# Optimization experiments

Measured on AMD Instinct MI355X. Metric: run time of the kernel, lower is better.

Reference implementation:

```python
import jax, jax.numpy as jnp
import numpy as np

B, N, D, H = 2, 2048, 1024, 16
DH = D // H  # 64 per-head dim before LRPE
EPS = 1e-5


def setup_inputs() -> dict:
    key = jax.random.key(0)
    ks = jax.random.split(key, 8)
    x = jax.random.normal(ks[0], (B, N, D), dtype=jnp.float32)
    context = jax.random.normal(ks[1], (B, N, D), dtype=jnp.float32)
    Wqkvu = jax.random.normal(ks[2], (4 * D, D), dtype=jnp.float32) * 0.02
    bqkvu = jax.random.normal(ks[3], (4 * D,), dtype=jnp.float32) * 0.02
    Wout = jax.random.normal(ks[4], (D, D), dtype=jnp.float32) * 0.02
    bout = jax.random.normal(ks[5], (D,), dtype=jnp.float32) * 0.02
    # Lrpe theta: 10000**(-2/d * arange(d)) reshaped to (H, 1, DH)
    theta = (10000.0 ** (-2.0 / D * jnp.arange(D, dtype=jnp.float32))).reshape(H, 1, DH)
    ln_w = jnp.ones((D,), dtype=jnp.float32)
    ln_b = jnp.zeros((D,), dtype=jnp.float32)
    return {"x": x, "context": context, "Wqkvu": Wqkvu, "bqkvu": bqkvu,
            "Wout": Wout, "bout": bout, "theta": theta, "ln_w": ln_w, "ln_b": ln_b}


def _lrpe(t, theta, n):
    # t: [b,h,n,d]; theta: [h,1,d]; index: [1,n,1]
    idx = jnp.arange(n, dtype=t.dtype).reshape(1, n, 1)
    th = theta * idx  # [h,n,d]
    return jnp.concatenate([t * jnp.cos(th), t * jnp.sin(th)], axis=-1)  # [b,h,n,2d]


def reference(x, context, Wqkvu, bqkvu, Wout, bout, theta, ln_w, ln_b):
    b, n, d = x.shape
    qkvu = x @ Wqkvu.T + bqkvu  # [b,n,4d]
    q, k, v, u = jnp.split(qkvu, 4, axis=-1)
    tohead = lambda t: t.reshape(b, n, H, DH).transpose(0, 2, 1, 3)  # b h n d
    q, k, v = tohead(q), tohead(k), tohead(v)
    q = jax.nn.silu(q)
    k = jax.nn.silu(k)
    q = _lrpe(q, theta, n)  # [b,h,n,2*DH]
    k = _lrpe(k, theta, n)
    # left form: materialize qk then contract with v
    qk = jnp.einsum('bhmd,bhnd->bhmn', q, k)
    out = jnp.einsum('bhmn,bhne->bhme', qk, v)  # [b,h,n,DH]
    out = out.transpose(0, 2, 1, 3).reshape(b, n, d)
    # LayerNorm
    mu = jnp.mean(out, axis=-1, keepdims=True)
    var = jnp.var(out, axis=-1, keepdims=True)
    out = (out - mu) * jax.lax.rsqrt(var + EPS) * ln_w + ln_b
    out = u * out
    return out @ Wout.T + bout
```

## Files before the change

kernel.cpp:

```cpp
#include <hip/hip_runtime.h>
#include <math.h>

#define B_ 2
#define N_ 2048
#define D_ 1024
#define H_ 16
#define DH_ 64
#define ROWS (B_*N_)
#define FOURD (4*D_)
#define EPS_ 1e-5f

typedef short bf16x8 __attribute__((ext_vector_type(8)));
typedef float f32x4  __attribute__((ext_vector_type(4)));

__device__ __forceinline__ unsigned short f2bf(float f) {
    unsigned int x = __float_as_uint(f);
    unsigned int r = (x + 0x7fffu + ((x >> 16) & 1u)) >> 16;
    return (unsigned short)r;
}

__global__ __launch_bounds__(256)
void cast_f32_bf16(const float* __restrict__ in, unsigned short* __restrict__ out, int n4)
{
    int i = blockIdx.x * 256 + threadIdx.x;
    if (i >= n4) return;
    float4 v = ((const float4*)in)[i];
    ushort4 o;
    o.x = f2bf(v.x); o.y = f2bf(v.y); o.z = f2bf(v.z); o.w = f2bf(v.w);
    ((ushort4*)out)[i] = o;
}

__global__ __launch_bounds__(256)
void gemm_bt_mfma(const unsigned short* __restrict__ A,
                  const unsigned short* __restrict__ Bw,
                  const float* __restrict__ bias, float* __restrict__ C,
                  int M, int N, int K, int siluLim)
{
    __shared__ unsigned short As[128 * 32];
    __shared__ unsigned short Bs[128 * 32];

    const int tid  = threadIdx.x;
    const int row0 = blockIdx.y * 128;
    const int col0 = blockIdx.x * 128;
    const int wave = tid >> 6;
    const int lane = tid & 63;
    const int wr   = (wave >> 1) * 64;
    const int wc   = (wave & 1) * 64;
    const int l15  = lane & 15;
    const int quad = lane >> 4;

    f32x4 acc[4][4] = {};

    const int srow = tid >> 2;
    const int skk  = (tid & 3) * 8;
    const unsigned short* ag = A  + (size_t)(row0 + srow) * K + skk;
    const unsigned short* bg = Bw + (size_t)(col0 + srow) * K + skk;

    typedef const __attribute__((address_space(1))) unsigned int* gp_t;
    typedef __attribute__((address_space(3))) unsigned int* lp_t;
    lp_t asd = (lp_t)(void*)&As[tid * 8];
    lp_t bsd = (lp_t)(void*)&Bs[tid * 8];

    for (int k0 = 0; k0 < K; k0 += 32) {
        __builtin_amdgcn_global_load_lds((gp_t)(const void*)(ag + k0),                asd,        16, 0, 0);
        __builtin_amdgcn_global_load_lds((gp_t)(const void*)(ag + (size_t)64*K + k0), asd + 1024, 16, 0, 0);
        __builtin_amdgcn_global_load_lds((gp_t)(const void*)(bg + k0),                bsd,        16, 0, 0);
        __builtin_amdgcn_global_load_lds((gp_t)(const void*)(bg + (size_t)64*K + k0), bsd + 1024, 16, 0, 0);
        __syncthreads();

        bf16x8 af[4], bfr[4];
#pragma unroll
        for (int i = 0; i < 4; ++i)
            af[i] = *(const bf16x8*)&As[(wr + i * 16 + l15) * 32 + quad * 8];
#pragma unroll
        for (int j = 0; j < 4; ++j)
            bfr[j] = *(const bf16x8*)&Bs[(wc + j * 16 + l15) * 32 + quad * 8];
#pragma unroll
        for (int i = 0; i < 4; ++i)
#pragma unroll
            for (int j = 0; j < 4; ++j)
                acc[i][j] = __builtin_amdgcn_mfma_f32_16x16x32_bf16(af[i], bfr[j], acc[i][j], 0, 0, 0);
        __syncthreads();
    }

#pragma unroll
    for (int i = 0; i < 4; ++i) {
        const int r0 = row0 + wr + i * 16 + quad * 4;
#pragma unroll
        for (int j = 0; j < 4; ++j) {
            const int c = col0 + wc + j * 16 + l15;
            const float bb = bias[c];
#pragma unroll
            for (int r = 0; r < 4; ++r) {
                float v = acc[i][j][r] + bb;
                if (c < siluLim) v = v / (1.f + expf(-v));
                C[(size_t)(r0 + r) * N + c] = v;
            }
        }
    }
}

__global__ __launch_bounds__(256)
void kv_mfma(const float* __restrict__ qkvu, const float* __restrict__ theta,
             float* __restrict__ part)
{
    __shared__ unsigned short kl_s[128][136];
    __shared__ unsigned short v_s [64][136];

    const int bid   = blockIdx.x;
    const int chunk = bid & 15;
    const int bh    = bid >> 4;
    const int h     = bh & 15;
    const int b     = bh >> 4;
    const int tid   = threadIdx.x;
    const int lane  = tid & 63;
    const int wave  = tid >> 6;
    const int l15   = lane & 15;
    const int quad  = lane >> 4;
    const int n0    = chunk * 128;

    for (int i = tid; i < 2048; i += 256) {
        const int nn  = i >> 4;
        const int dh0 = (i & 15) * 4;
        const int n   = n0 + nn;
        const float* qrow = qkvu + (size_t)(b * N_ + n) * FOURD;
        float4 k4 = *(const float4*)(qrow + D_     + h * DH_ + dh0);
        float4 v4 = *(const float4*)(qrow + 2 * D_ + h * DH_ + dh0);
        float kk[4] = {k4.x, k4.y, k4.z, k4.w};
        float vv[4] = {v4.x, v4.y, v4.z, v4.w};
#pragma unroll
        for (int j = 0; j < 4; ++j) {
            const int dh = dh0 + j;
            float s, c; sincosf(theta[h * DH_ + dh] * (float)n, &s, &c);
            kl_s[dh][nn]      = f2bf(kk[j] * c);
            kl_s[64 + dh][nn] = f2bf(kk[j] * s);
            v_s[dh][nn]       = f2bf(vv[j]);
        }
    }
    __syncthreads();

    f32x4 acc[2][4] = {};
#pragma unroll
    for (int ks = 0; ks < 4; ++ks) {
        bf16x8 a0 = *(const bf16x8*)&kl_s[wave * 32 +      l15][ks * 32 + quad * 8];
        bf16x8 a1 = *(const bf16x8*)&kl_s[wave * 32 + 16 + l15][ks * 32 + quad * 8];
#pragma unroll
        for (int j = 0; j < 4; ++j) {
            bf16x8 bfr = *(const bf16x8*)&v_s[j * 16 + l15][ks * 32 + quad * 8];
            acc[0][j] = __builtin_amdgcn_mfma_f32_16x16x32_bf16(a0, bfr, acc[0][j], 0, 0, 0);
            acc[1][j] = __builtin_amdgcn_mfma_f32_16x16x32_bf16(a1, bfr, acc[1][j], 0, 0, 0);
        }
    }

    float* pp = part + ((size_t)bh * 16 + chunk) * 8192;
#pragma unroll
    for (int i = 0; i < 2; ++i) {
        const int d0 = wave * 32 + i * 16 + quad * 4;
#pragma unroll
        for (int j = 0; j < 4; ++j) {
            const int e = j * 16 + l15;
#pragma unroll
            for (int r = 0; r < 4; ++r)
                pp[(d0 + r) * 64 + e] = acc[i][j][r];
        }
    }
}

__global__ __launch_bounds__(256)
void kv_reduce(const float* __restrict__ part, float* __restrict__ kv)
{
    const int i  = blockIdx.x * 256 + threadIdx.x;
    const int bh = i >> 13;
    const float* pp = part + ((size_t)bh * 16) * 8192 + (i & 8191);
    float s = 0.f;
#pragma unroll
    for (int c = 0; c < 16; ++c) s += pp[c * 8192];
    kv[i] = s;
}

__global__ __launch_bounds__(256)
void attn_ln_kernel(const float* __restrict__ qkvu, const float* __restrict__ kvb,
                    const float* __restrict__ theta, const float* __restrict__ ln_w,
                    const float* __restrict__ ln_b, unsigned short* __restrict__ g)
{
    __shared__ float qc_s[8][1024];
    __shared__ float qs_s[8][1024];
    __shared__ float red[4][16];
    __shared__ float mured[8], rsred[8];

    const int row0 = blockIdx.x * 8;
    const int b    = row0 >> 11;
    const int tid  = threadIdx.x;
    const int lane = tid & 63;
    const int wave = tid >> 6;

    for (int i = tid; i < 2048; i += 256) {
        const int r  = i >> 8;
        const int c0 = (i & 255) * 4;
        const int n  = (row0 + r) & (N_ - 1);
        float4 qv = *(const float4*)&qkvu[(size_t)(row0 + r) * FOURD + c0];
        float4 tv = *(const float4*)&theta[c0];
        float q[4] = {qv.x, qv.y, qv.z, qv.w};
        float t[4] = {tv.x, tv.y, tv.z, tv.w};
        float4 cv, sv;
        float* cp = (float*)&cv; float* sp = (float*)&sv;
#pragma unroll
        for (int j = 0; j < 4; ++j) {
            float s, c; sincosf(t[j] * (float)n, &s, &c);
            cp[j] = q[j] * c; sp[j] = q[j] * s;
        }
        *(float4*)&qc_s[r][c0] = cv;
        *(float4*)&qs_s[r][c0] = sv;
    }
    __syncthreads();

    const int c0 = tid * 4;
    const int h  = c0 >> 6;
    const int e0 = c0 & 63;
    const float* kvp = kvb + (size_t)(b * H_ + h) * 8192;

    float o[8][4] = {};
    for (int d = 0; d < 64; ++d) {
        float4 kc = *(const float4*)&kvp[d * 64 + e0];
        float4 ks = *(const float4*)&kvp[(64 + d) * 64 + e0];
#pragma unroll
        for (int r = 0; r < 8; ++r) {
            const float qc = qc_s[r][h * 64 + d];
            const float qs = qs_s[r][h * 64 + d];
            o[r][0] = fmaf(qc, kc.x, fmaf(qs, ks.x, o[r][0]));
            o[r][1] = fmaf(qc, kc.y, fmaf(qs, ks.y, o[r][1]));
            o[r][2] = fmaf(qc, kc.z, fmaf(qs, ks.z, o[r][2]));
            o[r][3] = fmaf(qc, kc.w, fmaf(qs, ks.w, o[r][3]));
        }
    }

    float sum[8], sq[8];
#pragma unroll
    for (int r = 0; r < 8; ++r) {
        sum[r] = o[r][0] + o[r][1] + o[r][2] + o[r][3];
        sq[r]  = o[r][0]*o[r][0] + o[r][1]*o[r][1] + o[r][2]*o[r][2] + o[r][3]*o[r][3];
    }
#pragma unroll
    for (int off = 32; off; off >>= 1)
#pragma unroll
        for (int r = 0; r < 8; ++r) {
            sum[r] += __shfl_down(sum[r], off, 64);
            sq[r]  += __shfl_down(sq[r],  off, 64);
        }
    if (lane == 0)
#pragma unroll
        for (int r = 0; r < 8; ++r) { red[wave][r] = sum[r]; red[wave][8 + r] = sq[r]; }
    __syncthreads();
    if (tid < 8) {
        const float s  = red[0][tid] + red[1][tid] + red[2][tid] + red[3][tid];
        const float q2 = red[0][8+tid] + red[1][8+tid] + red[2][8+tid] + red[3][8+tid];
        const float mu = s * (1.f / (float)D_);
        const float var = q2 * (1.f / (float)D_) - mu * mu;
        mured[tid] = mu;
        rsred[tid] = rsqrtf(var + EPS_);
    }
    __syncthreads();

    float4 wv = *(const float4*)&ln_w[c0];
    float4 bv = *(const float4*)&ln_b[c0];
#pragma unroll
    for (int r = 0; r < 8; ++r) {
        float4 uv = *(const float4*)&qkvu[(size_t)(row0 + r) * FOURD + 3 * D_ + c0];
        const float mu = mured[r], rs = rsred[r];
        ushort4 ov;
        ov.x = f2bf(((o[r][0] - mu) * rs * wv.x + bv.x) * uv.x);
        ov.y = f2bf(((o[r][1] - mu) * rs * wv.y + bv.y) * uv.y);
        ov.z = f2bf(((o[r][2] - mu) * rs * wv.z + bv.z) * uv.z);
        ov.w = f2bf(((o[r][3] - mu) * rs * wv.w + bv.w) * uv.w);
        *(ushort4*)&g[(size_t)(row0 + r) * D_ + c0] = ov;
    }
}

extern "C" void kernel_launch(void* const* d_in, const int* in_sizes, int n_in,
                              void* d_out, int out_size, void* d_ws, size_t ws_size,
                              hipStream_t stream)
{
    const float* x     = (const float*)d_in[0];
    const float* Wqkvu = (const float*)d_in[2];
    const float* bqkvu = (const float*)d_in[3];
    const float* Wout  = (const float*)d_in[4];
    const float* bout  = (const float*)d_in[5];
    const float* theta = (const float*)d_in[6];
    const float* ln_w  = (const float*)d_in[7];
    const float* ln_b  = (const float*)d_in[8];
    float* out = (float*)d_out;

    char* ws = (char*)d_ws;
    float*          qkvu  = (float*)ws;          ws += (size_t)ROWS * FOURD * 4;
    float*          kvbuf = (float*)ws;          ws += (size_t)B_ * H_ * 8192 * 4;
    unsigned short* wqb   = (unsigned short*)ws; ws += (size_t)FOURD * D_ * 2;
    unsigned short* wob   = (unsigned short*)ws; ws += (size_t)D_ * D_ * 2;
    unsigned short* xb    = (unsigned short*)ws; ws += (size_t)ROWS * D_ * 2;
    float*          part  = (float*)ws;
    unsigned short* gb    = (unsigned short*)ws;

    dim3 blk(256);
    cast_f32_bf16<<<dim3(ROWS * D_ / 4 / 256), blk, 0, stream>>>(x, xb, ROWS * D_ / 4);
    cast_f32_bf16<<<dim3(FOURD * D_ / 4 / 256), blk, 0, stream>>>(Wqkvu, wqb, FOURD * D_ / 4);
    cast_f32_bf16<<<dim3(D_ * D_ / 4 / 256), blk, 0, stream>>>(Wout, wob, D_ * D_ / 4);

    gemm_bt_mfma<<<dim3(FOURD / 128, ROWS / 128), blk, 0, stream>>>(
        xb, wqb, bqkvu, qkvu, ROWS, FOURD, D_, 2 * D_);
    kv_mfma<<<dim3(32 * 16), blk, 0, stream>>>(qkvu, theta, part);
    kv_reduce<<<dim3(32 * 8192 / 256), blk, 0, stream>>>(part, kvbuf);
    attn_ln_kernel<<<dim3(ROWS / 8), blk, 0, stream>>>(qkvu, kvbuf, theta, ln_w, ln_b, gb);
    gemm_bt_mfma<<<dim3(D_ / 128, ROWS / 128), blk, 0, stream>>>(
        gb, wob, bout, out, ROWS, D_, D_, 0);
}
```

Measured before the change: 242.4 us.

## Store QKVU intermediate in bf16 and use 128x64 tiles for output GEMM

The first GEMM now writes the qkvu intermediate as bf16 instead of fp32, halving its write traffic and the reads in kv_mfma and attn_ln_kernel, which now convert from bf16 on load. The output projection uses a new 128x64-tile GEMM, which doubles its grid from 256 to 512 blocks so the CUs are better filled. The trade-off is lower precision on q, k, v and u before the linear attention and LayerNorm.

```diff
diff --git a/kernel.cpp b/kernel.cpp
--- a/kernel.cpp
+++ b/kernel.cpp
@@ -11,12 +11,16 @@
 #define EPS_ 1e-5f
 
 typedef short bf16x8 __attribute__((ext_vector_type(8)));
+typedef unsigned short u16x8 __attribute__((ext_vector_type(8)));
 typedef float f32x4  __attribute__((ext_vector_type(4)));
 
 __device__ __forceinline__ unsigned short f2bf(float f) {
     unsigned int x = __float_as_uint(f);
     unsigned int r = (x + 0x7fffu + ((x >> 16) & 1u)) >> 16;
     return (unsigned short)r;
+}
+__device__ __forceinline__ float bf2f(unsigned short u) {
+    return __uint_as_float((unsigned int)u << 16);
 }
 
 __global__ __launch_bounds__(256)
@@ -31,10 +35,10 @@
 }
 
 __global__ __launch_bounds__(256)
-void gemm_bt_mfma(const unsigned short* __restrict__ A,
-                  const unsigned short* __restrict__ Bw,
-                  const float* __restrict__ bias, float* __restrict__ C,
-                  int M, int N, int K, int siluLim)
+void gemm_bt_128(const unsigned short* __restrict__ A,
+                 const unsigned short* __restrict__ Bw,
+                 const float* __restrict__ bias, unsigned short* __restrict__ C,
+                 int M, int N, int K, int siluLim)
 {
     __shared__ unsigned short As[128 * 32];
     __shared__ unsigned short Bs[128 * 32];
@@ -94,14 +98,79 @@
             for (int r = 0; r < 4; ++r) {
                 float v = acc[i][j][r] + bb;
                 if (c < siluLim) v = v / (1.f + expf(-v));
-                C[(size_t)(r0 + r) * N + c] = v;
+                C[(size_t)(r0 + r) * N + c] = f2bf(v);
             }
         }
     }
 }
 
 __global__ __launch_bounds__(256)
-void kv_mfma(const float* __restrict__ qkvu, const float* __restrict__ theta,
+void gemm_bt_64(const unsigned short* __restrict__ A,
+                const unsigned short* __restrict__ Bw,
+                const float* __restrict__ bias, float* __restrict__ C,
+                int M, int N, int K)
+{
+    __shared__ unsigned short As[128 * 32];
+    __shared__ unsigned short Bs[64 * 32];
+
+    const int tid  = threadIdx.x;
+    const int row0 = blockIdx.y * 128;
+    const int col0 = blockIdx.x * 64;
+    const int wave = tid >> 6;
+    const int lane = tid & 63;
+    const int wr   = wave * 32;
+    const int l15  = lane & 15;
+    const int quad = lane >> 4;
+
+    f32x4 acc[2][4] = {};
+
+    const int srow = tid >> 2;
+    const int skk  = (tid & 3) * 8;
+    const unsigned short* ag = A  + (size_t)(row0 + srow) * K + skk;
+    const unsigned short* bg = Bw + (size_t)(col0 + srow) * K + skk;
+
+    typedef const __attribute__((address_space(1))) unsigned int* gp_t;
+    typedef __attribute__((address_space(3))) unsigned int* lp_t;
+    lp_t asd = (lp_t)(void*)&As[tid * 8];
+    lp_t bsd = (lp_t)(void*)&Bs[tid * 8];
+
+    for (int k0 = 0; k0 < K; k0 += 32) {
+        __builtin_amdgcn_global_load_lds((gp_t)(const void*)(ag + k0),                asd,        16, 0, 0);
+        __builtin_amdgcn_global_load_lds((gp_t)(const void*)(ag + (size_t)64*K + k0), asd + 1024, 16, 0, 0);
+        __builtin_amdgcn_global_load_lds((gp_t)(const void*)(bg + k0),                bsd,        16, 0, 0);
+        __syncthreads();
+
+        bf16x8 af[2], bfr[4];
+#pragma unroll
+        for (int i = 0; i < 2; ++i)
+            af[i] = *(const bf16x8*)&As[(wr + i * 16 + l15) * 32 + quad * 8];
+#pragma unroll
+        for (int j = 0; j < 4; ++j)
+            bfr[j] = *(const bf16x8*)&Bs[(j * 16 + l15) * 32 + quad * 8];
+#pragma unroll
+        for (int i = 0; i < 2; ++i)
+#pragma unroll
+            for (int j = 0; j < 4; ++j)
+                acc[i][j] = __builtin_amdgcn_mfma_f32_16x16x32_bf16(af[i], bfr[j], acc[i][j], 0, 0, 0);
+        __syncthreads();
+    }
+
+#pragma unroll
+    for (int i = 0; i < 2; ++i) {
+        const int r0 = row0 + wr + i * 16 + quad * 4;
+#pragma unroll
+        for (int j = 0; j < 4; ++j) {
+            const int c = col0 + j * 16 + l15;
+            const float bb = bias[c];
+#pragma unroll
+            for (int r = 0; r < 4; ++r)
+                C[(size_t)(r0 + r) * N + c] = acc[i][j][r] + bb;
+        }
+    }
+}
+
+__global__ __launch_bounds__(256)
+void kv_mfma(const unsigned short* __restrict__ qkvu, const float* __restrict__ theta,
              float* __restrict__ part)
 {
     __shared__ unsigned short kl_s[128][136];
@@ -119,22 +188,21 @@
     const int quad  = lane >> 4;
     const int n0    = chunk * 128;
 
-    for (int i = tid; i < 2048; i += 256) {
-        const int nn  = i >> 4;
-        const int dh0 = (i & 15) * 4;
+    for (int i = tid; i < 1024; i += 256) {
+        const int nn  = i >> 3;
+        const int dh0 = (i & 7) * 8;
         const int n   = n0 + nn;
-        const float* qrow = qkvu + (size_t)(b * N_ + n) * FOURD;
-        float4 k4 = *(const float4*)(qrow + D_     + h * DH_ + dh0);
-        float4 v4 = *(const float4*)(qrow + 2 * D_ + h * DH_ + dh0);
-        float kk[4] = {k4.x, k4.y, k4.z, k4.w};
-        float vv[4] = {v4.x, v4.y, v4.z, v4.w};
-#pragma unroll
-        for (int j = 0; j < 4; ++j) {
+        const unsigned short* qrow = qkvu + (size_t)(b * N_ + n) * FOURD;
+        u16x8 k8 = *(const u16x8*)(qrow + D_     + h * DH_ + dh0);
+        u16x8 v8 = *(const u16x8*)(qrow + 2 * D_ + h * DH_ + dh0);
+#pragma unroll
+        for (int j = 0; j < 8; ++j) {
             const int dh = dh0 + j;
+            const float kf = bf2f(k8[j]);
             float s, c; sincosf(theta[h * DH_ + dh] * (float)n, &s, &c);
-            kl_s[dh][nn]      = f2bf(kk[j] * c);
-            kl_s[64 + dh][nn] = f2bf(kk[j] * s);
-            v_s[dh][nn]       = f2bf(vv[j]);
+            kl_s[dh][nn]      = f2bf(kf * c);
+            kl_s[64 + dh][nn] = f2bf(kf * s);
+            v_s[dh][nn]       = v8[j];
         }
     }
     __syncthreads();
@@ -179,7 +247,7 @@
 }
 
 __global__ __launch_bounds__(256)
-void attn_ln_kernel(const float* __restrict__ qkvu, const float* __restrict__ kvb,
+void attn_ln_kernel(const unsigned short* __restrict__ qkvu, const float* __restrict__ kvb,
                     const float* __restrict__ theta, const float* __restrict__ ln_w,
                     const float* __restrict__ ln_b, unsigned short* __restrict__ g)
 {
@@ -198,9 +266,9 @@
         const int r  = i >> 8;
         const int c0 = (i & 255) * 4;
         const int n  = (row0 + r) & (N_ - 1);
-        float4 qv = *(const float4*)&qkvu[(size_t)(row0 + r) * FOURD + c0];
+        ushort4 qv = *(const ushort4*)&qkvu[(size_t)(row0 + r) * FOURD + c0];
         float4 tv = *(const float4*)&theta[c0];
-        float q[4] = {qv.x, qv.y, qv.z, qv.w};
+        float q[4] = {bf2f(qv.x), bf2f(qv.y), bf2f(qv.z), bf2f(qv.w)};
         float t[4] = {tv.x, tv.y, tv.z, tv.w};
         float4 cv, sv;
         float* cp = (float*)&cv; float* sp = (float*)&sv;
@@ -265,13 +333,13 @@
     float4 bv = *(const float4*)&ln_b[c0];
 #pragma unroll
     for (int r = 0; r < 8; ++r) {
-        float4 uv = *(const float4*)&qkvu[(size_t)(row0 + r) * FOURD + 3 * D_ + c0];
+        ushort4 uvb = *(const ushort4*)&qkvu[(size_t)(row0 + r) * FOURD + 3 * D_ + c0];
         const float mu = mured[r], rs = rsred[r];
         ushort4 ov;
-        ov.x = f2bf(((o[r][0] - mu) * rs * wv.x + bv.x) * uv.x);
-        ov.y = f2bf(((o[r][1] - mu) * rs * wv.y + bv.y) * uv.y);
-        ov.z = f2bf(((o[r][2] - mu) * rs * wv.z + bv.z) * uv.z);
-        ov.w = f2bf(((o[r][3] - mu) * rs * wv.w + bv.w) * uv.w);
+        ov.x = f2bf(((o[r][0] - mu) * rs * wv.x + bv.x) * bf2f(uvb.x));
+        ov.y = f2bf(((o[r][1] - mu) * rs * wv.y + bv.y) * bf2f(uvb.y));
+        ov.z = f2bf(((o[r][2] - mu) * rs * wv.z + bv.z) * bf2f(uvb.z));
+        ov.w = f2bf(((o[r][3] - mu) * rs * wv.w + bv.w) * bf2f(uvb.w));
         *(ushort4*)&g[(size_t)(row0 + r) * D_ + c0] = ov;
     }
 }
@@ -291,7 +359,7 @@
     float* out = (float*)d_out;
 
     char* ws = (char*)d_ws;
-    float*          qkvu  = (float*)ws;          ws += (size_t)ROWS * FOURD * 4;
+    unsigned short* qkvu  = (unsigned short*)ws; ws += (size_t)ROWS * FOURD * 2;
     float*          kvbuf = (float*)ws;          ws += (size_t)B_ * H_ * 8192 * 4;
     unsigned short* wqb   = (unsigned short*)ws; ws += (size_t)FOURD * D_ * 2;
     unsigned short* wob   = (unsigned short*)ws; ws += (size_t)D_ * D_ * 2;
@@ -304,11 +372,11 @@
     cast_f32_bf16<<<dim3(FOURD * D_ / 4 / 256), blk, 0, stream>>>(Wqkvu, wqb, FOURD * D_ / 4);
     cast_f32_bf16<<<dim3(D_ * D_ / 4 / 256), blk, 0, stream>>>(Wout, wob, D_ * D_ / 4);
 
-    gemm_bt_mfma<<<dim3(FOURD / 128, ROWS / 128), blk, 0, stream>>>(
+    gemm_bt_128<<<dim3(FOURD / 128, ROWS / 128), blk, 0, stream>>>(
         xb, wqb, bqkvu, qkvu, ROWS, FOURD, D_, 2 * D_);
     kv_mfma<<<dim3(32 * 16), blk, 0, stream>>>(qkvu, theta, part);
     kv_reduce<<<dim3(32 * 8192 / 256), blk, 0, stream>>>(part, kvbuf);
     attn_ln_kernel<<<dim3(ROWS / 8), blk, 0, stream>>>(qkvu, kvbuf, theta, ln_w, ln_b, gb);
-    gemm_bt_mfma<<<dim3(D_ / 128, ROWS / 128), blk, 0, stream>>>(
-        gb, wob, bout, out, ROWS, D_, D_, 0);
-}
+    gemm_bt_64<<<dim3(D_ / 64, ROWS / 128), blk, 0, stream>>>(
+        gb, wob, bout, out, ROWS, D_, D_);
+}
```

Result: faster. 232.6 us (-4.0%).
